# Kernel tuning notes

Hardware: AMD Instinct MI355X
Metric: run time of the kernel (lower is better)

Reference implementation:

```python
import jax, jax.numpy as jnp
import numpy as np

R_SCALES = (1, 2, 4, 10, 25)
DIM = 300
B, L = 64, 800


def setup_inputs() -> dict:
    key = jax.random.key(0)
    k1, k2, k3 = jax.random.split(key, 3)
    inputs_c_e = jax.random.normal(k1, (B, L, DIM), dtype=jnp.float32)
    # xavier-normal-ish weights for the 5 per-scale Linear(DIM, DIM) layers
    std = float(np.sqrt(2.0 / (DIM + DIM)))
    W = jax.random.normal(k2, (5, DIM, DIM), dtype=jnp.float32) * std
    b = jax.random.normal(k3, (5, DIM), dtype=jnp.float32) * 0.01
    return {"inputs_c_e": inputs_c_e, "W": W, "b": b}


def _one_scale(x, W, bias, r):
    # x: [B, L, D]; W: [D, D] (torch Linear weight, y = x @ W.T + b)
    Bn, Ln, D = x.shape
    g = Ln // r
    rest = Ln - g * r
    # segment sum over groups of size r  -> [B, g, D]
    seg = x[:, : g * r].reshape(Bn, g, r, D).sum(axis=2)
    y = jax.nn.relu(jnp.einsum('bgd,ed->bge', seg, W) + bias) / r  # [B, g, D]
    y = jnp.repeat(y, r, axis=1)  # broadcast back to [B, g*r, D]
    if rest != 0:
        s = x[:, g * r:].sum(axis=1) * (r / rest)  # [B, D]
        yr = jax.nn.relu(s @ W.T + bias) / r       # [B, D]
        yr = jnp.broadcast_to(yr[:, None, :], (Bn, rest, D))
        y = jnp.concatenate([y, yr], axis=1)
    return y  # [B, L, D]


def reference(inputs_c_e, W, b):
    outs = [_one_scale(inputs_c_e, W[n], b[n], r) for n, r in enumerate(R_SCALES)]
    return jnp.stack(outs, axis=0)  # [5, B, L, D]
```

## Files before the change

### kernel.cpp

```cpp
#include <hip/hip_runtime.h>


typedef short bf16x8 __attribute__((ext_vector_type(8)));
typedef float f32x4  __attribute__((ext_vector_type(4)));

namespace {
constexpr int D    = 300;
constexpr int LSEQ = 800;
constexpr int KP   = 320;
constexpr int NP   = 320;
constexpr int CSTR = 308;
constexpr int SMEM_BYTES = 32 * CSTR * 4;
}

__device__ __forceinline__ unsigned short f2bf(float f) {
  unsigned u = __float_as_uint(f);
  u += 0x7fffu + ((u >> 16) & 1u);
  return (unsigned short)(u >> 16);
}

__global__ void convert_w(const float* __restrict__ W, short* __restrict__ Wb) {
  int idx = blockIdx.x * 256 + threadIdx.x;
  if (idx >= 5 * NP * KP) return;
  int n   = idx / (NP * KP);
  int rem = idx - n * (NP * KP);
  int c = rem / KP, k = rem - c * KP;
  float v = (c < D && k < D) ? W[(size_t)n * D * D + (size_t)c * D + k] : 0.f;
  Wb[idx] = (short)f2bf(v);
}

template<int N, int R, int G>
__device__ __forceinline__ void ce_body(const int tile, char* __restrict__ smem,
    const float* __restrict__ x, const short* __restrict__ Wb,
    const float* __restrict__ bias, float* __restrict__ out) {
  const int tid = threadIdx.x;
  const int m0  = tile * 32;
  constexpr int BQ = (R <= 5) ? R : 5;

  #pragma unroll
  for (int it = 0; it < 5; ++it) {
    const int cidx = tid + it * 256;
    const int row  = cidx / 40;
    const int k0   = (cidx - row * 40) * 8;
    float s[8];
    #pragma unroll
    for (int j = 0; j < 8; ++j) s[j] = 0.f;
    if (k0 < D) {
      const int m   = m0 + row;
      const int bb  = m / G;
      const int grp = m - bb * G;
      const float* xp = x + ((size_t)(bb * LSEQ + grp * R)) * D + k0;
      if (k0 <= D - 8) {
        for (int qb = 0; qb < R; qb += BQ) {
          float4 a0[BQ], a1[BQ];
          #pragma unroll
          for (int j = 0; j < BQ; ++j) {
            a0[j] = *(const float4*)(xp + (size_t)(qb + j) * D);
            a1[j] = *(const float4*)(xp + (size_t)(qb + j) * D + 4);
          }
          #pragma unroll
          for (int j = 0; j < BQ; ++j) {
            s[0] += a0[j].x; s[1] += a0[j].y; s[2] += a0[j].z; s[3] += a0[j].w;
            s[4] += a1[j].x; s[5] += a1[j].y; s[6] += a1[j].z; s[7] += a1[j].w;
          }
        }
      } else {
        for (int qb = 0; qb < R; qb += BQ) {
          float4 a0[BQ];
          #pragma unroll
          for (int j = 0; j < BQ; ++j)
            a0[j] = *(const float4*)(xp + (size_t)(qb + j) * D);
          #pragma unroll
          for (int j = 0; j < BQ; ++j) {
            s[0] += a0[j].x; s[1] += a0[j].y; s[2] += a0[j].z; s[3] += a0[j].w;
          }
        }
      }
    }
    bf16x8 p;
    #pragma unroll
    for (int j = 0; j < 8; ++j) p[j] = (short)f2bf(s[j]);
    const int boff = (row * 640 + k0 * 2) ^ ((row & 7) << 4);
    *(bf16x8*)(smem + boff) = p;
  }
  __syncthreads();

  const int wv   = tid >> 6;
  const int lane = tid & 63;
  const int cr   = lane & 15;
  const int kh   = lane >> 4;

  f32x4 acc[2][5];
  #pragma unroll
  for (int mt = 0; mt < 2; ++mt)
    #pragma unroll
    for (int t = 0; t < 5; ++t) acc[mt][t] = (f32x4){0.f, 0.f, 0.f, 0.f};

  const short* __restrict__ Wn = Wb + (size_t)N * NP * KP;
  const short* __restrict__ wp[5];
  #pragma unroll
  for (int t = 0; t < 5; ++t)
    wp[t] = Wn + (size_t)((wv * 5 + t) * 16 + cr) * KP + kh * 8;

  const int swz0 = (cr & 7) << 4;
  const int abase0 = cr * 640        + kh * 16;
  const int abase1 = (16 + cr) * 640 + kh * 16;

  bf16x8 bpre[5], a0pre, a1pre;
  #pragma unroll
  for (int t = 0; t < 5; ++t) bpre[t] = *(const bf16x8*)(wp[t]);
  a0pre = *(const bf16x8*)(smem + (abase0 ^ swz0));
  a1pre = *(const bf16x8*)(smem + (abase1 ^ swz0));

  #pragma unroll
  for (int ks = 0; ks < 10; ++ks) {
    bf16x8 bcur[5];
    #pragma unroll
    for (int t = 0; t < 5; ++t) bcur[t] = bpre[t];
    const bf16x8 a0 = a0pre, a1 = a1pre;
    if (ks < 9) {
      #pragma unroll
      for (int t = 0; t < 5; ++t) bpre[t] = *(const bf16x8*)(wp[t] + (ks + 1) * 32);
      a0pre = *(const bf16x8*)(smem + ((abase0 + (ks + 1) * 64) ^ swz0));
      a1pre = *(const bf16x8*)(smem + ((abase1 + (ks + 1) * 64) ^ swz0));
    }
    #pragma unroll
    for (int t = 0; t < 5; ++t) {
      acc[0][t] = __builtin_amdgcn_mfma_f32_16x16x32_bf16(a0, bcur[t], acc[0][t], 0, 0, 0);
      acc[1][t] = __builtin_amdgcn_mfma_f32_16x16x32_bf16(a1, bcur[t], acc[1][t], 0, 0, 0);
    }
  }
  __syncthreads();

  float* __restrict__ cout = (float*)smem;
  const float inv_r = 1.0f / (float)R;
  #pragma unroll
  for (int t = 0; t < 5; ++t) {
    const int col = (wv * 5 + t) * 16 + cr;
    if (col < D) {
      const float bv = bias[N * D + col];
      #pragma unroll
      for (int mt = 0; mt < 2; ++mt)
        #pragma unroll
        for (int j = 0; j < 4; ++j) {
          const int row = mt * 16 + kh * 4 + j;
          cout[row * CSTR + col] = fmaxf(acc[mt][t][j] + bv, 0.f) * inv_r;
        }
    }
  }
  __syncthreads();

  constexpr int TOTAL = 32 * R * 75;
  for (int i = tid; i < TOTAL; i += 256) {
    const int rowrep = i / 75;
    const int chunk  = i - rowrep * 75;
    const int ml     = rowrep / R;
    const int q      = rowrep - ml * R;
    const int m      = m0 + ml;
    const int bb     = m / G;
    const int grp    = m - bb * G;
    const f32x4 v = *(const f32x4*)(cout + ml * CSTR + chunk * 4);
    float* __restrict__ op =
        out + ((size_t)((N * 64 + bb) * LSEQ) + grp * R + q) * D + chunk * 4;
    *(f32x4*)op = v;
  }
}

__global__ __launch_bounds__(256, 4)
void ce_mfma8(const float* __restrict__ x, const short* __restrict__ Wb,
              const float* __restrict__ bias, float* __restrict__ out) {
  __shared__ __align__(16) char smem[SMEM_BYTES];
  const int bid = blockIdx.x;
  if (bid < 64)        ce_body<4, 25, 32 >(bid,        smem, x, Wb, bias, out);
  else if (bid < 224)  ce_body<3, 10, 80 >(bid - 64,   smem, x, Wb, bias, out);
  else if (bid < 624)  ce_body<2, 4, 200 >(bid - 224,  smem, x, Wb, bias, out);
  else if (bid < 1424) ce_body<1, 2, 400 >(bid - 624,  smem, x, Wb, bias, out);
  else                 ce_body<0, 1, 800 >(bid - 1424, smem, x, Wb, bias, out);
}

extern "C" void kernel_launch(void* const* d_in, const int* in_sizes, int n_in,
                              void* d_out, int out_size, void* d_ws, size_t ws_size,
                              hipStream_t stream) {
  const float* x    = (const float*)d_in[0];
  const float* W    = (const float*)d_in[1];
  const float* bias = (const float*)d_in[2];
  float* out        = (float*)d_out;
  short* Wb         = (short*)d_ws;

  convert_w<<<(5 * NP * KP + 255) / 256, 256, 0, stream>>>(W, Wb);
  ce_mfma8<<<3024, 256, 0, stream>>>(x, Wb, bias, out);
}
```

Before: 146.6 us.

## Double M tile to 64 rows per block to reuse weight fragments

Each block now handles 64 segment rows instead of 32, so every loaded weight fragment feeds four MFMA row tiles instead of two. This halves the weight traffic per output row and the grid size. The epilogue runs in two 32-row halves to reuse the shared buffer. The cost is more accumulator registers and larger shared memory, with launch bounds lowered to 3 blocks per CU, which reduces occupancy.

```diff
diff --git a/kernel.cpp b/kernel.cpp
--- a/kernel.cpp
+++ b/kernel.cpp
@@ -10,7 +10,9 @@
 constexpr int KP   = 320;
 constexpr int NP   = 320;
 constexpr int CSTR = 308;
-constexpr int SMEM_BYTES = 32 * CSTR * 4;
+constexpr int SEG_BYTES  = 64 * 640;
+constexpr int COUT_BYTES = 32 * CSTR * 4;
+constexpr int SMEM_BYTES = SEG_BYTES;
 }
 
 __device__ __forceinline__ unsigned short f2bf(float f) {
@@ -34,11 +36,11 @@
     const float* __restrict__ x, const short* __restrict__ Wb,
     const float* __restrict__ bias, float* __restrict__ out) {
   const int tid = threadIdx.x;
-  const int m0  = tile * 32;
+  const int m0  = tile * 64;
   constexpr int BQ = (R <= 5) ? R : 5;
 
   #pragma unroll
-  for (int it = 0; it < 5; ++it) {
+  for (int it = 0; it < 10; ++it) {
     const int cidx = tid + it * 256;
     const int row  = cidx / 40;
     const int k0   = (cidx - row * 40) * 8;
@@ -90,9 +92,9 @@
   const int cr   = lane & 15;
   const int kh   = lane >> 4;
 
-  f32x4 acc[2][5];
-  #pragma unroll
-  for (int mt = 0; mt < 2; ++mt)
+  f32x4 acc[4][5];
+  #pragma unroll
+  for (int mt = 0; mt < 4; ++mt)
     #pragma unroll
     for (int t = 0; t < 5; ++t) acc[mt][t] = (f32x4){0.f, 0.f, 0.f, 0.f};
 
@@ -102,80 +104,89 @@
   for (int t = 0; t < 5; ++t)
     wp[t] = Wn + (size_t)((wv * 5 + t) * 16 + cr) * KP + kh * 8;
 
-  const int swz0 = (cr & 7) << 4;
-  const int abase0 = cr * 640        + kh * 16;
-  const int abase1 = (16 + cr) * 640 + kh * 16;
-
-  bf16x8 bpre[5], a0pre, a1pre;
+  const int swz = (cr & 7) << 4;
+  int abase[4];
+  #pragma unroll
+  for (int mt = 0; mt < 4; ++mt) abase[mt] = (mt * 16 + cr) * 640 + kh * 16;
+
+  bf16x8 bpre[5], apre[4];
   #pragma unroll
   for (int t = 0; t < 5; ++t) bpre[t] = *(const bf16x8*)(wp[t]);
-  a0pre = *(const bf16x8*)(smem + (abase0 ^ swz0));
-  a1pre = *(const bf16x8*)(smem + (abase1 ^ swz0));
+  #pragma unroll
+  for (int mt = 0; mt < 4; ++mt)
+    apre[mt] = *(const bf16x8*)(smem + (abase[mt] ^ swz));
 
   #pragma unroll
   for (int ks = 0; ks < 10; ++ks) {
-    bf16x8 bcur[5];
+    bf16x8 bcur[5], acur[4];
     #pragma unroll
     for (int t = 0; t < 5; ++t) bcur[t] = bpre[t];
-    const bf16x8 a0 = a0pre, a1 = a1pre;
+    #pragma unroll
+    for (int mt = 0; mt < 4; ++mt) acur[mt] = apre[mt];
     if (ks < 9) {
       #pragma unroll
       for (int t = 0; t < 5; ++t) bpre[t] = *(const bf16x8*)(wp[t] + (ks + 1) * 32);
-      a0pre = *(const bf16x8*)(smem + ((abase0 + (ks + 1) * 64) ^ swz0));
-      a1pre = *(const bf16x8*)(smem + ((abase1 + (ks + 1) * 64) ^ swz0));
-    }
-    #pragma unroll
-    for (int t = 0; t < 5; ++t) {
-      acc[0][t] = __builtin_amdgcn_mfma_f32_16x16x32_bf16(a0, bcur[t], acc[0][t], 0, 0, 0);
-      acc[1][t] = __builtin_amdgcn_mfma_f32_16x16x32_bf16(a1, bcur[t], acc[1][t], 0, 0, 0);
-    }
+      #pragma unroll
+      for (int mt = 0; mt < 4; ++mt)
+        apre[mt] = *(const bf16x8*)(smem + ((abase[mt] + (ks + 1) * 64) ^ swz));
+    }
+    #pragma unroll
+    for (int t = 0; t < 5; ++t)
+      #pragma unroll
+      for (int mt = 0; mt < 4; ++mt)
+        acc[mt][t] = __builtin_amdgcn_mfma_f32_16x16x32_bf16(acur[mt], bcur[t], acc[mt][t], 0, 0, 0);
   }
   __syncthreads();
 
   float* __restrict__ cout = (float*)smem;
   const float inv_r = 1.0f / (float)R;
   #pragma unroll
-  for (int t = 0; t < 5; ++t) {
-    const int col = (wv * 5 + t) * 16 + cr;
-    if (col < D) {
-      const float bv = bias[N * D + col];
-      #pragma unroll
-      for (int mt = 0; mt < 2; ++mt)
+  for (int half = 0; half < 2; ++half) {
+    #pragma unroll
+    for (int t = 0; t < 5; ++t) {
+      const int col = (wv * 5 + t) * 16 + cr;
+      if (col < D) {
+        const float bv = bias[N * D + col];
         #pragma unroll
-        for (int j = 0; j < 4; ++j) {
-          const int row = mt * 16 + kh * 4 + j;
-          cout[row * CSTR + col] = fmaxf(acc[mt][t][j] + bv, 0.f) * inv_r;
-        }
-    }
+        for (int mt = 0; mt < 2; ++mt)
+          #pragma unroll
+          for (int j = 0; j < 4; ++j) {
+            const int row = mt * 16 + kh * 4 + j;
+            cout[row * CSTR + col] =
+                fmaxf(acc[half * 2 + mt][t][j] + bv, 0.f) * inv_r;
+          }
+      }
+    }
+    __syncthreads();
+
+    constexpr int TOTAL = 32 * R * 75;
+    for (int i = tid; i < TOTAL; i += 256) {
+      const int rowrep = i / 75;
+      const int chunk  = i - rowrep * 75;
+      const int ml     = rowrep / R;
+      const int q      = rowrep - ml * R;
+      const int m      = m0 + half * 32 + ml;
+      const int bb     = m / G;
+      const int grp    = m - bb * G;
+      const f32x4 v = *(const f32x4*)(cout + ml * CSTR + chunk * 4);
+      float* __restrict__ op =
+          out + ((size_t)((N * 64 + bb) * LSEQ) + grp * R + q) * D + chunk * 4;
+      *(f32x4*)op = v;
+    }
+    __syncthreads();
   }
-  __syncthreads();
-
-  constexpr int TOTAL = 32 * R * 75;
-  for (int i = tid; i < TOTAL; i += 256) {
-    const int rowrep = i / 75;
-    const int chunk  = i - rowrep * 75;
-    const int ml     = rowrep / R;
-    const int q      = rowrep - ml * R;
-    const int m      = m0 + ml;
-    const int bb     = m / G;
-    const int grp    = m - bb * G;
-    const f32x4 v = *(const f32x4*)(cout + ml * CSTR + chunk * 4);
-    float* __restrict__ op =
-        out + ((size_t)((N * 64 + bb) * LSEQ) + grp * R + q) * D + chunk * 4;
-    *(f32x4*)op = v;
-  }
-}
-
-__global__ __launch_bounds__(256, 4)
-void ce_mfma8(const float* __restrict__ x, const short* __restrict__ Wb,
+}
+
+__global__ __launch_bounds__(256, 3)
+void ce_mfma9(const float* __restrict__ x, const short* __restrict__ Wb,
               const float* __restrict__ bias, float* __restrict__ out) {
   __shared__ __align__(16) char smem[SMEM_BYTES];
   const int bid = blockIdx.x;
-  if (bid < 64)        ce_body<4, 25, 32 >(bid,        smem, x, Wb, bias, out);
-  else if (bid < 224)  ce_body<3, 10, 80 >(bid - 64,   smem, x, Wb, bias, out);
-  else if (bid < 624)  ce_body<2, 4, 200 >(bid - 224,  smem, x, Wb, bias, out);
-  else if (bid < 1424) ce_body<1, 2, 400 >(bid - 624,  smem, x, Wb, bias, out);
-  else                 ce_body<0, 1, 800 >(bid - 1424, smem, x, Wb, bias, out);
+  if (bid < 32)        ce_body<4, 25, 32 >(bid,        smem, x, Wb, bias, out);
+  else if (bid < 112)  ce_body<3, 10, 80 >(bid - 32,   smem, x, Wb, bias, out);
+  else if (bid < 312)  ce_body<2, 4, 200 >(bid - 112,  smem, x, Wb, bias, out);
+  else if (bid < 712)  ce_body<1, 2, 400 >(bid - 312,  smem, x, Wb, bias, out);
+  else                 ce_body<0, 1, 800 >(bid - 712,  smem, x, Wb, bias, out);
 }
 
 extern "C" void kernel_launch(void* const* d_in, const int* in_sizes, int n_in,
@@ -188,5 +199,5 @@
   short* Wb         = (short*)d_ws;
 
   convert_w<<<(5 * NP * KP + 255) / 256, 256, 0, stream>>>(W, Wb);
-  ce_mfma8<<<3024, 256, 0, stream>>>(x, Wb, bias, out);
-}
+  ce_mfma9<<<1512, 256, 0, stream>>>(x, Wb, bias, out);
+}
```

After: 150.0 us. 2.3% more time.
